# Performance work log

Measured on AMD Instinct MI355X. Metric: run time of the kernel, lower is better.

## Reference

```python
import jax, jax.numpy as jnp
import numpy as np

IN_CH, OUT_CH = 256, 128
HID = 2 * OUT_CH  # 256
N_NODES, N_EDGES = 50000, 800000


def setup_inputs() -> dict:
    key = jax.random.key(0)
    k1, k2, k3, k4, k5, k6, k7 = jax.random.split(key, 7)
    feats = jax.random.normal(k1, (N_NODES, IN_CH), dtype=jnp.float32)
    src = jax.random.randint(k2, (N_EDGES,), 0, N_NODES, dtype=jnp.int64)
    dst = jax.random.randint(k3, (N_EDGES,), 0, N_NODES, dtype=jnp.int64)
    # GraphConv weights: layer0 in->2*out, layer1 2*out->out (Glorot-ish scale)
    W0 = jax.random.normal(k4, (IN_CH, HID), dtype=jnp.float32) / np.sqrt(IN_CH)
    b0 = jnp.zeros((HID,), dtype=jnp.float32)
    W1 = jax.random.normal(k5, (HID, OUT_CH), dtype=jnp.float32) / np.sqrt(HID)
    b1 = jnp.zeros((OUT_CH,), dtype=jnp.float32)
    return {"feats": feats, "src": src, "dst": dst, "W0": W0, "b0": b0, "W1": W1, "b1": b1}


def _graph_conv(x, W, b, src, dst, norm_src, norm_dst, n_nodes):
    # Apply W first (out <= in) to shrink the edge-gather intermediate, as DGL does.
    h = x @ W                                  # [N, out]
    h = h * norm_src[:, None]                  # D_src^-1/2
    msg = h[src]                               # [E, out] irregular gather
    agg = jax.ops.segment_sum(msg, dst, num_segments=n_nodes)  # SpMM
    agg = agg * norm_dst[:, None] + b          # D_dst^-1/2, bias
    return jax.nn.relu(agg)


def reference(feats, src, dst, W0, b0, W1, b1):
    n = feats.shape[0]
    loop = jnp.arange(n, dtype=src.dtype)
    src_sl = jnp.concatenate([src, loop])      # dgl.add_self_loop
    dst_sl = jnpp = jnp.concatenate([dst, loop])
    ones = jnp.ones_like(src_sl, dtype=feats.dtype)
    out_deg = jax.ops.segment_sum(ones, src_sl, num_segments=n)
    in_deg = jax.ops.segment_sum(ones, dst_sl, num_segments=n)
    norm_src = jax.lax.rsqrt(jnp.maximum(out_deg, 1.0))
    norm_dst = jax.lax.rsqrt(jnp.maximum(in_deg, 1.0))
    x = _graph_conv(feats, W0, b0, src_sl, dst_sl, norm_src, norm_dst, n)
    x = _graph_conv(x, W1, b1, src_sl, dst_sl, norm_src, norm_dst, n)
    return x
```

## Files before the change

kernel.cpp:

```cpp
#include <hip/hip_runtime.h>


typedef __attribute__((ext_vector_type(8))) short short8v;
typedef __attribute__((ext_vector_type(4))) float float4v;
typedef __attribute__((ext_vector_type(8))) _Float16 half8v;
typedef __attribute__((ext_vector_type(4))) _Float16 half4v;
typedef __attribute__((ext_vector_type(2))) _Float16 half2v;

#define NSLAB 8
#define NCHUNK 32
#define MAXW 6272

__device__ inline unsigned short f2bf(float x) {
  unsigned u = __float_as_uint(x);
  return (unsigned short)((u + 0x7FFFu + ((u >> 16) & 1u)) >> 16);
}
__device__ inline float bf2f(unsigned short b) {
  return __uint_as_float(((unsigned)b) << 16);
}

__global__ __launch_bounds__(256) void k_histlds(
    const int* __restrict__ src, const int* __restrict__ dst,
    unsigned* __restrict__ cntO, unsigned* __restrict__ cntI,
    int W, int CE, int N, int E) {
  __shared__ unsigned ol[MAXW], il[MAXW];
  int s = blockIdx.x & (NSLAB - 1), c = blockIdx.x >> 3;
  int t = threadIdx.x;
  for (int i = t; i < W; i += 256) { ol[i] = 0u; il[i] = 0u; }
  __syncthreads();
  int sW = s * W;
  int e0 = c * CE, e1 = min(e0 + CE, E);
  for (int e = e0 + t; e < e1; e += 256) {
    int sv = src[e], dv = dst[e];
    unsigned so = (unsigned)(sv - sW);
    if (so < (unsigned)W) atomicAdd(&ol[so], 1u);
    unsigned dof = (unsigned)(dv - sW);
    if (dof < (unsigned)W) atomicAdd(&il[dof], 1u);
  }
  __syncthreads();
  int hi = min(W, N - sW);
  for (int i = t; i < hi; i += 256) {
    cntO[(size_t)c * N + sW + i] = ol[i];
    cntI[(size_t)c * N + sW + i] = il[i];
  }
}

__global__ __launch_bounds__(256) void k_scan1_norm(
    const unsigned* __restrict__ cntO, const unsigned* __restrict__ cntI,
    int* __restrict__ part, int* __restrict__ bsums,
    float* __restrict__ nsrc, float* __restrict__ ndst, int N) {
  __shared__ int s[256];
  int t = threadIdx.x, g = blockIdx.x * 256 + t;
  int od = 0, id = 0;
  if (g < N) {
#pragma unroll
    for (int c = 0; c < NCHUNK; ++c) {
      od += cntO[(size_t)c * N + g];
      id += cntI[(size_t)c * N + g];
    }
    nsrc[g] = rsqrtf((float)(od + 1));
    ndst[g] = rsqrtf((float)(id + 1));
  }
  int v = (g < N) ? id : 0;
  s[t] = v;
  __syncthreads();
  for (int o = 1; o < 256; o <<= 1) {
    int add = (t >= o) ? s[t - o] : 0;
    __syncthreads();
    s[t] += add;
    __syncthreads();
  }
  if (g < N) part[g] = s[t] - v;
  if (t == 255) bsums[blockIdx.x] = s[255];
}

__global__ __launch_bounds__(256) void k_scan23(
    int* __restrict__ part, int* __restrict__ cursor32,
    const int* __restrict__ bsums, const unsigned* __restrict__ cntI,
    int nb, int N, int E) {
  __shared__ int s[256];
  int t = threadIdx.x, g = blockIdx.x * 256 + t;
  int v = (t < nb) ? bsums[t] : 0;
  s[t] = v;
  __syncthreads();
  for (int o = 1; o < 256; o <<= 1) {
    int add = (t >= o) ? s[t - o] : 0;
    __syncthreads();
    s[t] += add;
    __syncthreads();
  }
  int off = s[blockIdx.x] - bsums[blockIdx.x];
  if (g < N) {
    int r = part[g] + off;
    part[g] = r;
    int run = r;
#pragma unroll
    for (int c = 0; c < NCHUNK; ++c) {
      cursor32[(size_t)c * N + g] = run;
      run += cntI[(size_t)c * N + g];
    }
  }
  if (g == 0) part[N] = E;
}

__global__ __launch_bounds__(256) void k_fill_lds(
    const int* __restrict__ src, const int* __restrict__ dst,
    const int* __restrict__ cursor32, int* __restrict__ colidx,
    int W, int CE, int N, int E) {
  __shared__ unsigned rl[MAXW];
  int s = blockIdx.x & (NSLAB - 1), c = blockIdx.x >> 3;
  int t = threadIdx.x;
  for (int i = t; i < W; i += 256) rl[i] = 0u;
  __syncthreads();
  int sW = s * W;
  int e0 = c * CE, e1 = min(e0 + CE, E);
  const int* cbase = cursor32 + (size_t)c * N;
  for (int e = e0 + t; e < e1; e += 256) {
    int sv = src[e], dv = dst[e];
    unsigned dof = (unsigned)(dv - sW);
    if (dof < (unsigned)W) {
      unsigned r = atomicAdd(&rl[dof], 1u);
      colidx[cbase[dv] + (int)r] = sv;
    }
  }
}

__global__ __launch_bounds__(256) void k_wsplit2(
    const float* __restrict__ W0, short* __restrict__ W0tH,
    short* __restrict__ W0tL, const float* __restrict__ W1,
    short* __restrict__ W1tH, short* __restrict__ W1tL) {
  const int K = 256, N0 = 256, N1 = 128;
  int idx = blockIdx.x * 256 + threadIdx.x;
  if (idx < K * N0) {
    int k = idx & (K - 1), n = idx >> 8;
    float v = W0[(size_t)k * N0 + n];
    unsigned short h = f2bf(v);
    W0tH[(size_t)n * K + k] = (short)h;
    W0tL[(size_t)n * K + k] = (short)f2bf(v - bf2f(h));
  } else {
    int j = idx - K * N0;
    if (j < K * N1) {
      int k = j & (K - 1), n = j >> 8;
      float v = W1[(size_t)k * N1 + n];
      unsigned short h = f2bf(v);
      W1tH[(size_t)n * K + k] = (short)h;
      W1tL[(size_t)n * K + k] = (short)f2bf(v - bf2f(h));
    }
  }
}

template <int NCOL, typename AT>
__global__ __launch_bounds__(256) void k_gemm_mfma(
    const AT* __restrict__ A, const short* __restrict__ WtH,
    const short* __restrict__ WtL, const float* __restrict__ norm,
    _Float16* __restrict__ out, int M) {
  constexpr int K = 256, BM = 64, BK = 32, PAD = 40, NF = NCOL / 16;
  __shared__ short AH[BM][PAD], AL[BM][PAD];
  __shared__ short BH[NCOL][PAD], BL[NCOL][PAD];
  int tid = threadIdx.x;
  int w = tid >> 6, l = tid & 63;
  int lg = l >> 4, ln = l & 15;
  int row0 = blockIdx.x * BM;

  float4v acc[NF];
#pragma unroll
  for (int i = 0; i < NF; ++i) acc[i] = (float4v){0.f, 0.f, 0.f, 0.f};

  int ar = tid >> 2;
  int akq = (tid & 3) * 8;

  for (int k0 = 0; k0 < K; k0 += BK) {
    float av[8];
    int grow = row0 + ar;
    if (grow < M) {
      if constexpr (sizeof(AT) == 4) {
        const float4* ap =
            reinterpret_cast<const float4*>(&A[(size_t)grow * K + k0 + akq]);
        float4 v0 = ap[0], v1 = ap[1];
        av[0] = v0.x; av[1] = v0.y; av[2] = v0.z; av[3] = v0.w;
        av[4] = v1.x; av[5] = v1.y; av[6] = v1.z; av[7] = v1.w;
      } else {
        half8v v =
            *reinterpret_cast<const half8v*>(&A[(size_t)grow * K + k0 + akq]);
#pragma unroll
        for (int i = 0; i < 8; ++i) av[i] = (float)v[i];
      }
    } else {
#pragma unroll
      for (int i = 0; i < 8; ++i) av[i] = 0.f;
    }
    short hh[8], ll[8];
#pragma unroll
    for (int i = 0; i < 8; ++i) {
      unsigned short h = f2bf(av[i]);
      hh[i] = (short)h;
      ll[i] = (short)f2bf(av[i] - bf2f(h));
    }
    *reinterpret_cast<short8v*>(&AH[ar][akq]) = *reinterpret_cast<short8v*>(hh);
    *reinterpret_cast<short8v*>(&AL[ar][akq]) = *reinterpret_cast<short8v*>(ll);

#pragma unroll
    for (int c = 0; c < NCOL / 64; ++c) {
      int chunk = c * 256 + tid;
      int bn = chunk >> 2, q = (chunk & 3) * 8;
      *reinterpret_cast<short8v*>(&BH[bn][q]) =
          *reinterpret_cast<const short8v*>(&WtH[(size_t)bn * K + k0 + q]);
      *reinterpret_cast<short8v*>(&BL[bn][q]) =
          *reinterpret_cast<const short8v*>(&WtL[(size_t)bn * K + k0 + q]);
    }
    __syncthreads();

    short8v aH = *reinterpret_cast<short8v*>(&AH[w * 16 + ln][lg * 8]);
    short8v aL = *reinterpret_cast<short8v*>(&AL[w * 16 + ln][lg * 8]);
#pragma unroll
    for (int nf = 0; nf < NF; ++nf) {
      short8v bHv = *reinterpret_cast<short8v*>(&BH[nf * 16 + ln][lg * 8]);
      short8v bLv = *reinterpret_cast<short8v*>(&BL[nf * 16 + ln][lg * 8]);
      acc[nf] = __builtin_amdgcn_mfma_f32_16x16x32_bf16(aH, bHv, acc[nf], 0, 0, 0);
      acc[nf] = __builtin_amdgcn_mfma_f32_16x16x32_bf16(aH, bLv, acc[nf], 0, 0, 0);
      acc[nf] = __builtin_amdgcn_mfma_f32_16x16x32_bf16(aL, bHv, acc[nf], 0, 0, 0);
    }
    __syncthreads();
  }

  int rbase = row0 + w * 16 + lg * 4;
  float nrm[4];
#pragma unroll
  for (int j = 0; j < 4; ++j)
    nrm[j] = (rbase + j < M) ? norm[rbase + j] : 0.f;
#pragma unroll
  for (int nf = 0; nf < NF; ++nf) {
#pragma unroll
    for (int j = 0; j < 4; ++j) {
      int r = rbase + j;
      if (r < M)
        out[(size_t)r * NCOL + nf * 16 + ln] = (_Float16)(acc[nf][j] * nrm[j]);
    }
  }
}

__global__ __launch_bounds__(256) void k_agg256(
    const _Float16* __restrict__ h, const int* __restrict__ rowptr,
    const int* __restrict__ colidx, const float* __restrict__ nd,
    const float* __restrict__ bias, _Float16* __restrict__ out, int N) {
  int node = blockIdx.x * 4 + (threadIdx.x >> 6);
  int lane = threadIdx.x & 63;
  if (node >= N) return;
  const half4v* hv = reinterpret_cast<const half4v*>(h);
  half4v hs = hv[(size_t)node * 64 + lane];
  float4 acc;
  acc.x = (float)hs[0]; acc.y = (float)hs[1];
  acc.z = (float)hs[2]; acc.w = (float)hs[3];
  int e0 = rowptr[node], e1 = rowptr[node + 1];
  int e = e0;
  for (; e + 7 < e1; e += 8) {
    int si[8];
#pragma unroll
    for (int i = 0; i < 8; ++i) si[i] = colidx[e + i];
    half4v v[8];
#pragma unroll
    for (int i = 0; i < 8; ++i) v[i] = hv[(size_t)si[i] * 64 + lane];
#pragma unroll
    for (int i = 0; i < 8; ++i) {
      acc.x += (float)v[i][0]; acc.y += (float)v[i][1];
      acc.z += (float)v[i][2]; acc.w += (float)v[i][3];
    }
  }
  for (; e < e1; ++e) {
    half4v v0 = hv[(size_t)colidx[e] * 64 + lane];
    acc.x += (float)v0[0]; acc.y += (float)v0[1];
    acc.z += (float)v0[2]; acc.w += (float)v0[3];
  }
  float n = nd[node];
  float4 b = reinterpret_cast<const float4*>(bias)[lane];
  half4v r = {(_Float16)fmaxf(fmaf(acc.x, n, b.x), 0.f),
              (_Float16)fmaxf(fmaf(acc.y, n, b.y), 0.f),
              (_Float16)fmaxf(fmaf(acc.z, n, b.z), 0.f),
              (_Float16)fmaxf(fmaf(acc.w, n, b.w), 0.f)};
  reinterpret_cast<half4v*>(out)[(size_t)node * 64 + lane] = r;
}

__global__ __launch_bounds__(256) void k_agg128(
    const _Float16* __restrict__ h, const int* __restrict__ rowptr,
    const int* __restrict__ colidx, const float* __restrict__ nd,
    const float* __restrict__ bias, float* __restrict__ out, int N) {
  int node = blockIdx.x * 4 + (threadIdx.x >> 6);
  int lane = threadIdx.x & 63;
  if (node >= N) return;
  const half2v* hv = reinterpret_cast<const half2v*>(h);
  half2v hs = hv[(size_t)node * 64 + lane];
  float2 acc;
  acc.x = (float)hs[0]; acc.y = (float)hs[1];
  int e0 = rowptr[node], e1 = rowptr[node + 1];
  int e = e0;
  for (; e + 7 < e1; e += 8) {
    int si[8];
#pragma unroll
    for (int i = 0; i < 8; ++i) si[i] = colidx[e + i];
    half2v v[8];
#pragma unroll
    for (int i = 0; i < 8; ++i) v[i] = hv[(size_t)si[i] * 64 + lane];
#pragma unroll
    for (int i = 0; i < 8; ++i) {
      acc.x += (float)v[i][0]; acc.y += (float)v[i][1];
    }
  }
  for (; e < e1; ++e) {
    half2v v0 = hv[(size_t)colidx[e] * 64 + lane];
    acc.x += (float)v0[0]; acc.y += (float)v0[1];
  }
  float n = nd[node];
  float2 b = reinterpret_cast<const float2*>(bias)[lane];
  float2 r;
  r.x = fmaxf(fmaf(acc.x, n, b.x), 0.f);
  r.y = fmaxf(fmaf(acc.y, n, b.y), 0.f);
  reinterpret_cast<float2*>(out)[(size_t)node * 64 + lane] = r;
}

extern "C" void kernel_launch(void* const* d_in, const int* in_sizes, int n_in,
                              void* d_out, int out_size, void* d_ws, size_t ws_size,
                              hipStream_t stream) {
  const float* feats = (const float*)d_in[0];
  const int* src = (const int*)d_in[1];
  const int* dst = (const int*)d_in[2];
  const float* W0 = (const float*)d_in[3];
  const float* b0 = (const float*)d_in[4];
  const float* W1 = (const float*)d_in[5];
  const float* b1 = (const float*)d_in[6];
  float* out = (float*)d_out;

  const int IN_CH = 256, HID = 256, OUT_CH = 128;
  int N = in_sizes[0] / IN_CH;
  int E = in_sizes[1];
  int W = (N + NSLAB - 1) / NSLAB;
  int CE = (E + NCHUNK - 1) / NCHUNK;

  char* ws = (char*)d_ws;
  size_t off = 0;
  auto alloc = [&](size_t bytes) -> void* {
    void* p = ws + off;
    off += (bytes + 255) & ~(size_t)255;
    return p;
  };
  _Float16* h0 = (_Float16*)alloc((size_t)N * HID * 2);
  _Float16* x1 = (_Float16*)alloc((size_t)N * HID * 2);
  float* nsrc   = (float*)alloc((size_t)N * 4);
  float* ndst   = (float*)alloc((size_t)N * 4);
  unsigned* cntO = (unsigned*)alloc((size_t)NCHUNK * N * 4);
  unsigned* cntI = (unsigned*)alloc((size_t)NCHUNK * N * 4);
  int*   rowptr = (int*)alloc((size_t)(N + 1) * 4);
  int* cursor32 = (int*)alloc((size_t)NCHUNK * N * 4);
  int*   colidx = (int*)alloc((size_t)E * 4);
  int*   bsums  = (int*)alloc(1024);
  short* w0h    = (short*)alloc((size_t)HID * IN_CH * 2);
  short* w0l    = (short*)alloc((size_t)HID * IN_CH * 2);
  short* w1h    = (short*)alloc((size_t)OUT_CH * HID * 2);
  short* w1l    = (short*)alloc((size_t)OUT_CH * HID * 2);
  _Float16* h1  = h0;

  int nbN = (N + 255) / 256;
  k_histlds<<<NSLAB * NCHUNK, 256, 0, stream>>>(src, dst, cntO, cntI, W, CE, N, E);
  k_scan1_norm<<<nbN, 256, 0, stream>>>(cntO, cntI, rowptr, bsums, nsrc, ndst, N);
  k_scan23<<<nbN, 256, 0, stream>>>(rowptr, cursor32, bsums, cntI, nbN, N, E);
  k_fill_lds<<<NSLAB * NCHUNK, 256, 0, stream>>>(src, dst, cursor32, colidx, W, CE, N, E);

  k_wsplit2<<<(IN_CH * HID + HID * OUT_CH) / 256, 256, 0, stream>>>(
      W0, w0h, w0l, W1, w1h, w1l);

  int gm = (N + 63) / 64;
  k_gemm_mfma<256, float><<<gm, 256, 0, stream>>>(feats, w0h, w0l, nsrc, h0, N);
  k_agg256<<<(N + 3) / 4, 256, 0, stream>>>(h0, rowptr, colidx, ndst, b0, x1, N);

  k_gemm_mfma<128, _Float16><<<gm, 256, 0, stream>>>(x1, w1h, w1l, nsrc, h1, N);
  k_agg128<<<(N + 3) / 4, 256, 0, stream>>>(h1, rowptr, colidx, ndst, b1, out, N);
}
```

Measured before the change: 377.0 us.

## Switch GEMM to 32x32x16 MFMA with 2x2 wave tiling

Replaces the 16x16x32 bf16 MFMA tiling, where each wave owned 16 rows by all columns, with 32x32x16 MFMA tiles. The four waves are arranged 2x2 so each owns 32 rows by half the columns. This is meant to cut LDS reads of the B operand per MFMA and improve operand reuse. It raises accumulator register pressure (16 floats per tile) and changes the epilogue store pattern.

```diff
diff --git a/kernel.cpp b/kernel.cpp
--- a/kernel.cpp
+++ b/kernel.cpp
@@ -2,7 +2,7 @@
 
 
 typedef __attribute__((ext_vector_type(8))) short short8v;
-typedef __attribute__((ext_vector_type(4))) float float4v;
+typedef __attribute__((ext_vector_type(16))) float float16v;
 typedef __attribute__((ext_vector_type(8))) _Float16 half8v;
 typedef __attribute__((ext_vector_type(4))) _Float16 half4v;
 typedef __attribute__((ext_vector_type(2))) _Float16 half2v;
@@ -154,17 +154,22 @@
     const AT* __restrict__ A, const short* __restrict__ WtH,
     const short* __restrict__ WtL, const float* __restrict__ norm,
     _Float16* __restrict__ out, int M) {
-  constexpr int K = 256, BM = 64, BK = 32, PAD = 40, NF = NCOL / 16;
+  constexpr int K = 256, BM = 64, BK = 32, PAD = 40;
+  constexpr int WCOLS = NCOL / 2;
+  constexpr int NCF = WCOLS / 32;
   __shared__ short AH[BM][PAD], AL[BM][PAD];
   __shared__ short BH[NCOL][PAD], BL[NCOL][PAD];
   int tid = threadIdx.x;
-  int w = tid >> 6, l = tid & 63;
-  int lg = l >> 4, ln = l & 15;
+  int wid = tid >> 6, l = tid & 63;
+  int wr = wid >> 1, wc = wid & 1;
+  int l31 = l & 31, lh = l >> 5;
   int row0 = blockIdx.x * BM;
 
-  float4v acc[NF];
-#pragma unroll
-  for (int i = 0; i < NF; ++i) acc[i] = (float4v){0.f, 0.f, 0.f, 0.f};
+  float16v acc[NCF];
+#pragma unroll
+  for (int i = 0; i < NCF; ++i)
+#pragma unroll
+    for (int j = 0; j < 16; ++j) acc[i][j] = 0.f;
 
   int ar = tid >> 2;
   int akq = (tid & 3) * 8;
@@ -210,31 +215,38 @@
     }
     __syncthreads();
 
-    short8v aH = *reinterpret_cast<short8v*>(&AH[w * 16 + ln][lg * 8]);
-    short8v aL = *reinterpret_cast<short8v*>(&AL[w * 16 + ln][lg * 8]);
-#pragma unroll
-    for (int nf = 0; nf < NF; ++nf) {
-      short8v bHv = *reinterpret_cast<short8v*>(&BH[nf * 16 + ln][lg * 8]);
-      short8v bLv = *reinterpret_cast<short8v*>(&BL[nf * 16 + ln][lg * 8]);
-      acc[nf] = __builtin_amdgcn_mfma_f32_16x16x32_bf16(aH, bHv, acc[nf], 0, 0, 0);
-      acc[nf] = __builtin_amdgcn_mfma_f32_16x16x32_bf16(aH, bLv, acc[nf], 0, 0, 0);
-      acc[nf] = __builtin_amdgcn_mfma_f32_16x16x32_bf16(aL, bHv, acc[nf], 0, 0, 0);
-    }
-    __syncthreads();
-  }
-
-  int rbase = row0 + w * 16 + lg * 4;
-  float nrm[4];
-#pragma unroll
-  for (int j = 0; j < 4; ++j)
-    nrm[j] = (rbase + j < M) ? norm[rbase + j] : 0.f;
-#pragma unroll
-  for (int nf = 0; nf < NF; ++nf) {
-#pragma unroll
-    for (int j = 0; j < 4; ++j) {
-      int r = rbase + j;
-      if (r < M)
-        out[(size_t)r * NCOL + nf * 16 + ln] = (_Float16)(acc[nf][j] * nrm[j]);
+#pragma unroll
+    for (int ks = 0; ks < 2; ++ks) {
+      short8v aH = *reinterpret_cast<short8v*>(&AH[wr * 32 + l31][ks * 16 + lh * 8]);
+      short8v aL = *reinterpret_cast<short8v*>(&AL[wr * 32 + l31][ks * 16 + lh * 8]);
+#pragma unroll
+      for (int cf = 0; cf < NCF; ++cf) {
+        int bi = wc * WCOLS + cf * 32 + l31;
+        short8v bH = *reinterpret_cast<short8v*>(&BH[bi][ks * 16 + lh * 8]);
+        short8v bL = *reinterpret_cast<short8v*>(&BL[bi][ks * 16 + lh * 8]);
+        acc[cf] = __builtin_amdgcn_mfma_f32_32x32x16_bf16(aH, bH, acc[cf], 0, 0, 0);
+        acc[cf] = __builtin_amdgcn_mfma_f32_32x32x16_bf16(aH, bL, acc[cf], 0, 0, 0);
+        acc[cf] = __builtin_amdgcn_mfma_f32_32x32x16_bf16(aL, bH, acc[cf], 0, 0, 0);
+      }
+    }
+    __syncthreads();
+  }
+
+  int rbase = row0 + wr * 32 + 4 * lh;
+  float nrm[16];
+#pragma unroll
+  for (int r = 0; r < 16; ++r) {
+    int row = rbase + (r & 3) + 8 * (r >> 2);
+    nrm[r] = (row < M) ? norm[row] : 0.f;
+  }
+#pragma unroll
+  for (int cf = 0; cf < NCF; ++cf) {
+    int col = wc * WCOLS + cf * 32 + l31;
+#pragma unroll
+    for (int r = 0; r < 16; ++r) {
+      int row = rbase + (r & 3) + 8 * (r >> 2);
+      if (row < M)
+        out[(size_t)row * NCOL + col] = (_Float16)(acc[cf][r] * nrm[r]);
     }
   }
 }
```

Measured after the change: 371.2 us. Within noise of the previous version (-1.5%).
